# Optimization experiments

Measured on AMD Instinct MI355X. Metric: run time of the kernel, lower is better.

## Reference

```python
import jax, jax.numpy as jnp
import numpy as np

N_NODES = 50000
N_EDGES = 800000
D_FEAT = 128


def setup_inputs() -> dict:
    key = jax.random.key(0)
    k1, k2, k3, k4 = jax.random.split(key, 4)
    x = jax.random.normal(k1, (N_NODES, D_FEAT), dtype=jnp.float32)
    vals = jax.random.uniform(k2, (N_EDGES,), dtype=jnp.float32)
    rows = jnp.sort(jax.random.randint(k3, (N_EDGES,), 0, N_NODES, dtype=jnp.int32))
    cols = jax.random.randint(k4, (N_EDGES,), 0, N_NODES, dtype=jnp.int32)
    return {"x": x, "vals": vals, "rows": rows, "cols": cols}


def reference(x, vals, rows, cols):
    # out = A @ x where A is sparse COO: out[r] += vals[e] * x[cols[e]] for each edge e with rows[e]==r
    messages = vals[:, None] * x[cols]  # [E, d]
    out = jax.ops.segment_sum(messages, rows, num_segments=N_NODES)  # [N, d]
    return out
```

## Files before the change

### kernel.cpp

```cpp
#include <hip/hip_runtime.h>


#define D_FEAT 128
#define TOTAL_WAVES 8192
#define WAVES_PER_BLOCK 4
#define BLOCK_THREADS (WAVES_PER_BLOCK * 64)
#define PF 8

typedef float v2f __attribute__((ext_vector_type(2)));

__device__ __forceinline__ float bcast_f(float v, int j) {
    return __int_as_float(__builtin_amdgcn_readlane(__float_as_int(v), j));
}

__device__ __forceinline__ unsigned short f2bf_rne(float f) {
    unsigned int b = __float_as_uint(f);
    b += 0x7fffu + ((b >> 16) & 1u);
    return (unsigned short)(b >> 16);
}

__global__ __launch_bounds__(256) void to_bf16_kernel(
    const float* __restrict__ x, unsigned short* __restrict__ xb, int n4) {
    const float4* __restrict__ x4 = (const float4*)x;
    ushort4* __restrict__ o4 = (ushort4*)xb;
    for (int i = blockIdx.x * blockDim.x + threadIdx.x; i < n4;
         i += gridDim.x * blockDim.x) {
        float4 f = x4[i];
        ushort4 o;
        o.x = f2bf_rne(f.x);
        o.y = f2bf_rne(f.y);
        o.z = f2bf_rne(f.z);
        o.w = f2bf_rne(f.w);
        o4[i] = o;
    }
}

__global__ __launch_bounds__(BLOCK_THREADS) void agg_bf16_kernel(
    const unsigned int* __restrict__ xb,
    const float* __restrict__ vals, const int* __restrict__ rows,
    const int* __restrict__ cols, float* __restrict__ out, int n_edges,
    int epw) {
    const int wave = blockIdx.x * WAVES_PER_BLOCK + (threadIdx.x >> 6);
    const int lane = threadIdx.x & 63;

    const int start = wave * epw;
    if (start >= n_edges) return;
    int end = start + epw;
    if (end > n_edges) end = n_edges;

    const int first_row = rows[start];
    const int last_row  = rows[end - 1];

    float2 acc = make_float2(0.f, 0.f);
    int cur_row = first_row;

    for (int e0 = start; e0 < end; e0 += 64) {
        const int nb = min(end - e0, 64);
        int myc = 0, myr = 0;
        float myv = 0.f;
        if (lane < nb) {
            myc = __builtin_nontemporal_load(cols + e0 + lane);
            myr = __builtin_nontemporal_load(rows + e0 + lane);
            myv = __builtin_nontemporal_load(vals + e0 + lane);
        }
        for (int j0 = 0; j0 < nb; j0 += PF) {
            const int m = min(nb - j0, PF);
            unsigned int xu[PF];
            int   rj[PF];
            float vj[PF];
#pragma unroll
            for (int t = 0; t < PF; ++t) {
                if (t < m) {
                    const int cj = __builtin_amdgcn_readlane(myc, j0 + t);
                    rj[t] = __builtin_amdgcn_readlane(myr, j0 + t);
                    vj[t] = bcast_f(myv, j0 + t);
                    xu[t] = xb[(size_t)cj * (D_FEAT / 2) + lane];
                }
            }
#pragma unroll
            for (int t = 0; t < PF; ++t) {
                if (t < m) {
                    if (rj[t] != cur_row) {
                        float* o = out + (size_t)cur_row * D_FEAT + 2 * lane;
                        if (cur_row == first_row || cur_row == last_row) {
                            atomicAdd(o,     acc.x);
                            atomicAdd(o + 1, acc.y);
                        } else {
                            v2f st; st.x = acc.x; st.y = acc.y;
                            __builtin_nontemporal_store(st, (v2f*)o);
                        }
                        acc.x = 0.f; acc.y = 0.f;
                        cur_row = rj[t];
                    }
                    const float x0 = __uint_as_float(xu[t] << 16);
                    const float x1 = __uint_as_float(xu[t] & 0xffff0000u);
                    acc.x = fmaf(vj[t], x0, acc.x);
                    acc.y = fmaf(vj[t], x1, acc.y);
                }
            }
        }
    }
    float* o = out + (size_t)cur_row * D_FEAT + 2 * lane;
    atomicAdd(o,     acc.x);
    atomicAdd(o + 1, acc.y);
}

__global__ __launch_bounds__(BLOCK_THREADS) void agg_f32_kernel(
    const float* __restrict__ x, const float* __restrict__ vals,
    const int* __restrict__ rows, const int* __restrict__ cols,
    float* __restrict__ out, int n_edges, int epw) {
    const int wave = blockIdx.x * WAVES_PER_BLOCK + (threadIdx.x >> 6);
    const int lane = threadIdx.x & 63;

    const int start = wave * epw;
    if (start >= n_edges) return;
    int end = start + epw;
    if (end > n_edges) end = n_edges;

    const float2* __restrict__ x2 = (const float2*)x;
    const int first_row = rows[start];
    const int last_row  = rows[end - 1];

    float2 acc = make_float2(0.f, 0.f);
    int cur_row = first_row;

    for (int e0 = start; e0 < end; e0 += 64) {
        const int nb = min(end - e0, 64);
        int myc = 0, myr = 0;
        float myv = 0.f;
        if (lane < nb) {
            myc = __builtin_nontemporal_load(cols + e0 + lane);
            myr = __builtin_nontemporal_load(rows + e0 + lane);
            myv = __builtin_nontemporal_load(vals + e0 + lane);
        }
        for (int j0 = 0; j0 < nb; j0 += PF) {
            const int m = min(nb - j0, PF);
            float2 xv[PF];
            int    rj[PF];
            float  vj[PF];
#pragma unroll
            for (int t = 0; t < PF; ++t) {
                if (t < m) {
                    const int cj = __builtin_amdgcn_readlane(myc, j0 + t);
                    rj[t] = __builtin_amdgcn_readlane(myr, j0 + t);
                    vj[t] = bcast_f(myv, j0 + t);
                    xv[t] = x2[(size_t)cj * (D_FEAT / 2) + lane];
                }
            }
#pragma unroll
            for (int t = 0; t < PF; ++t) {
                if (t < m) {
                    if (rj[t] != cur_row) {
                        float* o = out + (size_t)cur_row * D_FEAT + 2 * lane;
                        if (cur_row == first_row || cur_row == last_row) {
                            atomicAdd(o,     acc.x);
                            atomicAdd(o + 1, acc.y);
                        } else {
                            v2f st; st.x = acc.x; st.y = acc.y;
                            __builtin_nontemporal_store(st, (v2f*)o);
                        }
                        acc.x = 0.f; acc.y = 0.f;
                        cur_row = rj[t];
                    }
                    acc.x = fmaf(vj[t], xv[t].x, acc.x);
                    acc.y = fmaf(vj[t], xv[t].y, acc.y);
                }
            }
        }
    }
    float* o = out + (size_t)cur_row * D_FEAT + 2 * lane;
    atomicAdd(o,     acc.x);
    atomicAdd(o + 1, acc.y);
}

extern "C" void kernel_launch(void* const* d_in, const int* in_sizes, int n_in,
                              void* d_out, int out_size, void* d_ws, size_t ws_size,
                              hipStream_t stream) {
    const float* x    = (const float*)d_in[0];
    const float* vals = (const float*)d_in[1];
    const int*   rows = (const int*)d_in[2];
    const int*   cols = (const int*)d_in[3];
    float*       out  = (float*)d_out;

    const int n_edges = in_sizes[1];
    const int n_x     = in_sizes[0];

    (void)hipMemsetAsync(d_out, 0, (size_t)out_size * sizeof(float), stream);

    const int epw    = (n_edges + TOTAL_WAVES - 1) / TOTAL_WAVES;
    const int blocks = TOTAL_WAVES / WAVES_PER_BLOCK;

    const size_t need = (size_t)n_x * sizeof(unsigned short);
    if (ws_size >= need) {
        unsigned short* xb = (unsigned short*)d_ws;
        to_bf16_kernel<<<2048, 256, 0, stream>>>(x, xb, n_x / 4);
        agg_bf16_kernel<<<blocks, BLOCK_THREADS, 0, stream>>>(
            (const unsigned int*)xb, vals, rows, cols, out, n_edges, epw);
    } else {
        agg_f32_kernel<<<blocks, BLOCK_THREADS, 0, stream>>>(
            x, vals, rows, cols, out, n_edges, epw);
    }
}
```

Measured before the change: 126.9 us.

## Build CSR row pointers in prep kernel, align wave ranges to rows, drop atomics and memset

The prep kernel now also builds a CSR row_ptr array from the sorted rows and zeroes only the empty output rows. This replaces the full-output memset. The aggregation kernel binary-searches row_ptr so that each wave owns whole rows, which lets every output row be written with a plain nontemporal store instead of atomics at the wave boundaries. The cost is extra work in the prep kernel, a binary search per wave, and some load imbalance when a row is long.

Result: slower. 131.2 us (+3.4%).

```diff
diff --git a/kernel.cpp b/kernel.cpp
--- a/kernel.cpp
+++ b/kernel.cpp
@@ -19,12 +19,15 @@
     return (unsigned short)(b >> 16);
 }
 
-__global__ __launch_bounds__(256) void to_bf16_kernel(
-    const float* __restrict__ x, unsigned short* __restrict__ xb, int n4) {
+__global__ __launch_bounds__(256) void prep_kernel(
+    const float* __restrict__ x, const int* __restrict__ rows,
+    unsigned short* __restrict__ xb, int* __restrict__ row_ptr,
+    float* __restrict__ out, int n4, int n_edges, int n_nodes) {
+    const int tid = blockIdx.x * blockDim.x + threadIdx.x;
+    const int nth = gridDim.x * blockDim.x;
     const float4* __restrict__ x4 = (const float4*)x;
     ushort4* __restrict__ o4 = (ushort4*)xb;
-    for (int i = blockIdx.x * blockDim.x + threadIdx.x; i < n4;
-         i += gridDim.x * blockDim.x) {
+    for (int i = tid; i < n4; i += nth) {
         float4 f = x4[i];
         ushort4 o;
         o.x = f2bf_rne(f.x);
@@ -33,26 +36,53 @@
         o.w = f2bf_rne(f.w);
         o4[i] = o;
     }
+    for (int e = tid; e <= n_edges; e += nth) {
+        int r, rp;
+        if (e < n_edges) {
+            r  = rows[e];
+            rp = (e == 0) ? -1 : rows[e - 1];
+        } else {
+            r  = n_nodes;
+            rp = rows[n_edges - 1];
+        }
+        for (int q = rp + 1; q <= r; ++q)
+            if (q <= n_nodes) row_ptr[q] = e;
+        for (int q = rp + 1; q < r && q < n_nodes; ++q) {
+            float4* zo = (float4*)(out + (size_t)q * D_FEAT);
+            for (int k = 0; k < D_FEAT / 4; ++k) zo[k] = make_float4(0.f, 0.f, 0.f, 0.f);
+        }
+    }
 }
 
 __global__ __launch_bounds__(BLOCK_THREADS) void agg_bf16_kernel(
     const unsigned int* __restrict__ xb,
     const float* __restrict__ vals, const int* __restrict__ rows,
-    const int* __restrict__ cols, float* __restrict__ out, int n_edges,
-    int epw) {
+    const int* __restrict__ cols, const int* __restrict__ row_ptr,
+    float* __restrict__ out, int n_edges, int n_nodes, int epw) {
     const int wave = blockIdx.x * WAVES_PER_BLOCK + (threadIdx.x >> 6);
     const int lane = threadIdx.x & 63;
 
-    const int start = wave * epw;
-    if (start >= n_edges) return;
-    int end = start + epw;
-    if (end > n_edges) end = n_edges;
-
-    const int first_row = rows[start];
-    const int last_row  = rows[end - 1];
-
+    const int s = wave * epw;
+    if (s >= n_edges) return;
+    const int s2 = min(s + epw, n_edges);
+
+    int lo = 0, hi = n_nodes;
+    while (lo < hi) {
+        int mid = (lo + hi) >> 1;
+        if (row_ptr[mid] < s) lo = mid + 1; else hi = mid;
+    }
+    const int r_lo = lo;
+    hi = n_nodes;
+    while (lo < hi) {
+        int mid = (lo + hi) >> 1;
+        if (row_ptr[mid] < s2) lo = mid + 1; else hi = mid;
+    }
+    const int start = row_ptr[r_lo];
+    const int end   = row_ptr[lo];
+    if (start >= end) return;
+
+    int cur_row = rows[start];
     float2 acc = make_float2(0.f, 0.f);
-    int cur_row = first_row;
 
     for (int e0 = start; e0 < end; e0 += 64) {
         const int nb = min(end - e0, 64);
@@ -81,14 +111,9 @@
             for (int t = 0; t < PF; ++t) {
                 if (t < m) {
                     if (rj[t] != cur_row) {
-                        float* o = out + (size_t)cur_row * D_FEAT + 2 * lane;
-                        if (cur_row == first_row || cur_row == last_row) {
-                            atomicAdd(o,     acc.x);
-                            atomicAdd(o + 1, acc.y);
-                        } else {
-                            v2f st; st.x = acc.x; st.y = acc.y;
-                            __builtin_nontemporal_store(st, (v2f*)o);
-                        }
+                        v2f st; st.x = acc.x; st.y = acc.y;
+                        __builtin_nontemporal_store(
+                            st, (v2f*)(out + (size_t)cur_row * D_FEAT + 2 * lane));
                         acc.x = 0.f; acc.y = 0.f;
                         cur_row = rj[t];
                     }
@@ -100,9 +125,8 @@
             }
         }
     }
-    float* o = out + (size_t)cur_row * D_FEAT + 2 * lane;
-    atomicAdd(o,     acc.x);
-    atomicAdd(o + 1, acc.y);
+    v2f st; st.x = acc.x; st.y = acc.y;
+    __builtin_nontemporal_store(st, (v2f*)(out + (size_t)cur_row * D_FEAT + 2 * lane));
 }
 
 __global__ __launch_bounds__(BLOCK_THREADS) void agg_f32_kernel(
@@ -129,9 +153,9 @@
         int myc = 0, myr = 0;
         float myv = 0.f;
         if (lane < nb) {
-            myc = __builtin_nontemporal_load(cols + e0 + lane);
-            myr = __builtin_nontemporal_load(rows + e0 + lane);
-            myv = __builtin_nontemporal_load(vals + e0 + lane);
+            myc = cols[e0 + lane];
+            myr = rows[e0 + lane];
+            myv = vals[e0 + lane];
         }
         for (int j0 = 0; j0 < nb; j0 += PF) {
             const int m = min(nb - j0, PF);
@@ -184,19 +208,25 @@
 
     const int n_edges = in_sizes[1];
     const int n_x     = in_sizes[0];
-
-    (void)hipMemsetAsync(d_out, 0, (size_t)out_size * sizeof(float), stream);
+    const int n_nodes = out_size / D_FEAT;
 
     const int epw    = (n_edges + TOTAL_WAVES - 1) / TOTAL_WAVES;
     const int blocks = TOTAL_WAVES / WAVES_PER_BLOCK;
 
-    const size_t need = (size_t)n_x * sizeof(unsigned short);
+    const size_t xb_bytes = (size_t)n_x * sizeof(unsigned short);
+    const size_t rp_off   = (xb_bytes + 255) & ~(size_t)255;
+    const size_t need     = rp_off + (size_t)(n_nodes + 1) * sizeof(int);
+
     if (ws_size >= need) {
         unsigned short* xb = (unsigned short*)d_ws;
-        to_bf16_kernel<<<2048, 256, 0, stream>>>(x, xb, n_x / 4);
+        int* row_ptr = (int*)((char*)d_ws + rp_off);
+        prep_kernel<<<2048, 256, 0, stream>>>(x, rows, xb, row_ptr, out,
+                                              n_x / 4, n_edges, n_nodes);
         agg_bf16_kernel<<<blocks, BLOCK_THREADS, 0, stream>>>(
-            (const unsigned int*)xb, vals, rows, cols, out, n_edges, epw);
+            (const unsigned int*)xb, vals, rows, cols, row_ptr, out,
+            n_edges, n_nodes, epw);
     } else {
+        (void)hipMemsetAsync(d_out, 0, (size_t)out_size * sizeof(float), stream);
         agg_f32_kernel<<<blocks, BLOCK_THREADS, 0, stream>>>(
             x, vals, rows, cols, out, n_edges, epw);
     }
```

## Pack column index and bf16 value into one word; ballot-based row boundaries

Applied to the files above, without the earlier changes.

The prep kernel now also packs each edge's column index (16 bits) and its value rounded to bf16 into a single 32-bit word. The aggregation kernel therefore reads two streams instead of three. Row boundaries are found with one shuffle-and-ballot per 64-edge chunk, which removes the per-edge row comparisons and the partial-chunk masking. Edges per wave are fixed at 128, giving more, shorter waves. This adds requirements that node count fit in 16 bits and that the edge count be a multiple of 64, and it loses precision on vals by rounding them to bf16. The prep kernel also has more work to do.

Result: faster. 119.8 us (median of 2 runs) (-5.6%).

```diff
diff --git a/kernel.cpp b/kernel.cpp
--- a/kernel.cpp
+++ b/kernel.cpp
@@ -2,9 +2,9 @@
 
 
 #define D_FEAT 128
-#define TOTAL_WAVES 8192
+#define EPW 128
 #define WAVES_PER_BLOCK 4
-#define BLOCK_THREADS (WAVES_PER_BLOCK * 64)
+#define BLOCK_THREADS 256
 #define PF 8
 
 typedef float v2f __attribute__((ext_vector_type(2)));
@@ -19,12 +19,15 @@
     return (unsigned short)(b >> 16);
 }
 
-__global__ __launch_bounds__(256) void to_bf16_kernel(
-    const float* __restrict__ x, unsigned short* __restrict__ xb, int n4) {
+__global__ __launch_bounds__(256) void prep_kernel(
+    const float* __restrict__ x, const float* __restrict__ vals,
+    const int* __restrict__ cols, unsigned short* __restrict__ xb,
+    unsigned int* __restrict__ cv, int n4, int n_edges) {
+    const int tid = blockIdx.x * blockDim.x + threadIdx.x;
+    const int nth = gridDim.x * blockDim.x;
     const float4* __restrict__ x4 = (const float4*)x;
     ushort4* __restrict__ o4 = (ushort4*)xb;
-    for (int i = blockIdx.x * blockDim.x + threadIdx.x; i < n4;
-         i += gridDim.x * blockDim.x) {
+    for (int i = tid; i < n4; i += nth) {
         float4 f = x4[i];
         ushort4 o;
         o.x = f2bf_rne(f.x);
@@ -33,75 +36,77 @@
         o.w = f2bf_rne(f.w);
         o4[i] = o;
     }
+    for (int e = tid; e < n_edges; e += nth) {
+        cv[e] = ((unsigned int)cols[e] << 16) | (unsigned int)f2bf_rne(vals[e]);
+    }
 }
 
 __global__ __launch_bounds__(BLOCK_THREADS) void agg_bf16_kernel(
     const unsigned int* __restrict__ xb,
-    const float* __restrict__ vals, const int* __restrict__ rows,
-    const int* __restrict__ cols, float* __restrict__ out, int n_edges,
-    int epw) {
+    const unsigned int* __restrict__ cv,
+    const int* __restrict__ rows, float* __restrict__ out, int n_edges) {
     const int wave = blockIdx.x * WAVES_PER_BLOCK + (threadIdx.x >> 6);
     const int lane = threadIdx.x & 63;
 
-    const int start = wave * epw;
+    const int start = wave * EPW;
     if (start >= n_edges) return;
-    int end = start + epw;
-    if (end > n_edges) end = n_edges;
+    const int end = min(start + EPW, n_edges);
 
     const int first_row = rows[start];
-    const int last_row  = rows[end - 1];
-
     float2 acc = make_float2(0.f, 0.f);
     int cur_row = first_row;
 
     for (int e0 = start; e0 < end; e0 += 64) {
-        const int nb = min(end - e0, 64);
-        int myc = 0, myr = 0;
-        float myv = 0.f;
-        if (lane < nb) {
-            myc = __builtin_nontemporal_load(cols + e0 + lane);
-            myr = __builtin_nontemporal_load(rows + e0 + lane);
-            myv = __builtin_nontemporal_load(vals + e0 + lane);
-        }
-        for (int j0 = 0; j0 < nb; j0 += PF) {
-            const int m = min(nb - j0, PF);
+        const unsigned int mycv = __builtin_nontemporal_load(cv + e0 + lane);
+        const int myr = __builtin_nontemporal_load(rows + e0 + lane);
+        const int nxt = __shfl(myr, (lane + 1) & 63);
+        const unsigned long long bmask =
+            __ballot(myr != nxt) & 0x7fffffffffffffffULL;
+        const int g0 = __builtin_amdgcn_readfirstlane(myr);
+        if (g0 != cur_row) {
+            float* o = out + (size_t)cur_row * D_FEAT + 2 * lane;
+            if (cur_row == first_row) {
+                atomicAdd(o, acc.x);
+                atomicAdd(o + 1, acc.y);
+            } else {
+                v2f st; st.x = acc.x; st.y = acc.y;
+                __builtin_nontemporal_store(st, (v2f*)o);
+            }
+            acc.x = 0.f; acc.y = 0.f;
+            cur_row = g0;
+        }
+#pragma unroll
+        for (int j0 = 0; j0 < 64; j0 += PF) {
+            unsigned int sv[PF];
             unsigned int xu[PF];
-            int   rj[PF];
-            float vj[PF];
-#pragma unroll
-            for (int t = 0; t < PF; ++t) {
-                if (t < m) {
-                    const int cj = __builtin_amdgcn_readlane(myc, j0 + t);
-                    rj[t] = __builtin_amdgcn_readlane(myr, j0 + t);
-                    vj[t] = bcast_f(myv, j0 + t);
-                    xu[t] = xb[(size_t)cj * (D_FEAT / 2) + lane];
+#pragma unroll
+            for (int t = 0; t < PF; ++t) {
+                sv[t] = (unsigned int)__builtin_amdgcn_readlane((int)mycv, j0 + t);
+                xu[t] = xb[(size_t)(sv[t] >> 16) * (D_FEAT / 2) + lane];
+            }
+#pragma unroll
+            for (int t = 0; t < PF; ++t) {
+                const float vf = __uint_as_float(sv[t] << 16);
+                acc.x = fmaf(vf, __uint_as_float(xu[t] << 16), acc.x);
+                acc.y = fmaf(vf, __uint_as_float(xu[t] & 0xffff0000u), acc.y);
+                if ((bmask >> (j0 + t)) & 1ULL) {
+                    const int fr = __builtin_amdgcn_readlane(myr, j0 + t);
+                    float* o = out + (size_t)fr * D_FEAT + 2 * lane;
+                    if (fr == first_row) {
+                        atomicAdd(o, acc.x);
+                        atomicAdd(o + 1, acc.y);
+                    } else {
+                        v2f st; st.x = acc.x; st.y = acc.y;
+                        __builtin_nontemporal_store(st, (v2f*)o);
+                    }
+                    acc.x = 0.f; acc.y = 0.f;
                 }
             }
-#pragma unroll
-            for (int t = 0; t < PF; ++t) {
-                if (t < m) {
-                    if (rj[t] != cur_row) {
-                        float* o = out + (size_t)cur_row * D_FEAT + 2 * lane;
-                        if (cur_row == first_row || cur_row == last_row) {
-                            atomicAdd(o,     acc.x);
-                            atomicAdd(o + 1, acc.y);
-                        } else {
-                            v2f st; st.x = acc.x; st.y = acc.y;
-                            __builtin_nontemporal_store(st, (v2f*)o);
-                        }
-                        acc.x = 0.f; acc.y = 0.f;
-                        cur_row = rj[t];
-                    }
-                    const float x0 = __uint_as_float(xu[t] << 16);
-                    const float x1 = __uint_as_float(xu[t] & 0xffff0000u);
-                    acc.x = fmaf(vj[t], x0, acc.x);
-                    acc.y = fmaf(vj[t], x1, acc.y);
-                }
-            }
-        }
+        }
+        cur_row = __builtin_amdgcn_readlane(myr, 63);
     }
     float* o = out + (size_t)cur_row * D_FEAT + 2 * lane;
-    atomicAdd(o,     acc.x);
+    atomicAdd(o, acc.x);
     atomicAdd(o + 1, acc.y);
 }
 
@@ -129,9 +134,9 @@
         int myc = 0, myr = 0;
         float myv = 0.f;
         if (lane < nb) {
-            myc = __builtin_nontemporal_load(cols + e0 + lane);
-            myr = __builtin_nontemporal_load(rows + e0 + lane);
-            myv = __builtin_nontemporal_load(vals + e0 + lane);
+            myc = cols[e0 + lane];
+            myr = rows[e0 + lane];
+            myv = vals[e0 + lane];
         }
         for (int j0 = 0; j0 < nb; j0 += PF) {
             const int m = min(nb - j0, PF);
@@ -184,19 +189,30 @@
 
     const int n_edges = in_sizes[1];
     const int n_x     = in_sizes[0];
+    const int n_nodes = out_size / D_FEAT;
 
     (void)hipMemsetAsync(d_out, 0, (size_t)out_size * sizeof(float), stream);
 
-    const int epw    = (n_edges + TOTAL_WAVES - 1) / TOTAL_WAVES;
-    const int blocks = TOTAL_WAVES / WAVES_PER_BLOCK;
-
-    const size_t need = (size_t)n_x * sizeof(unsigned short);
-    if (ws_size >= need) {
+    const size_t xb_bytes = (size_t)n_x * sizeof(unsigned short);
+    const size_t cv_off   = (xb_bytes + 255) & ~(size_t)255;
+    const size_t need     = cv_off + (size_t)n_edges * sizeof(unsigned int);
+
+    const bool fast_ok = (ws_size >= need) && (n_edges % 64 == 0) &&
+                         (n_nodes <= 65536) && (n_x % 4 == 0);
+
+    if (fast_ok) {
         unsigned short* xb = (unsigned short*)d_ws;
-        to_bf16_kernel<<<2048, 256, 0, stream>>>(x, xb, n_x / 4);
+        unsigned int*   cv = (unsigned int*)((char*)d_ws + cv_off);
+        prep_kernel<<<2048, 256, 0, stream>>>(x, vals, cols, xb, cv,
+                                              n_x / 4, n_edges);
+        const int waves  = (n_edges + EPW - 1) / EPW;
+        const int blocks = (waves + WAVES_PER_BLOCK - 1) / WAVES_PER_BLOCK;
         agg_bf16_kernel<<<blocks, BLOCK_THREADS, 0, stream>>>(
-            (const unsigned int*)xb, vals, rows, cols, out, n_edges, epw);
+            (const unsigned int*)xb, cv, rows, out, n_edges);
     } else {
+        const int total_waves = 8192;
+        const int epw    = (n_edges + total_waves - 1) / total_waves;
+        const int blocks = total_waves / WAVES_PER_BLOCK;
         agg_f32_kernel<<<blocks, BLOCK_THREADS, 0, stream>>>(
             x, vals, rows, cols, out, n_edges, epw);
     }
```
